# Performance work log

Measured on AMD Instinct MI355X. Metric: run time of the kernel, lower is better.

Reference implementation:

```python
import jax, jax.numpy as jnp
import numpy as np

B, S, E = 2, 2048, 2048
H, D = 16, 128  # num_attention_heads, head_dim = hidden_size // num_heads


def rotate_half(x):
    x1 = x[..., : x.shape[-1] // 2]
    x2 = x[..., x.shape[-1] // 2 :]
    return jnp.concatenate((-x2, x1), axis=-1)


def setup_inputs() -> dict:
    key = jax.random.key(0)
    ks = jax.random.split(key, 7)
    return {
        "hidden_states": jax.random.normal(ks[0], (B, S, E), dtype=jnp.float32),
        "cos": jax.random.uniform(ks[1], (1, 1, S, D), dtype=jnp.float32),
        "sin": jax.random.uniform(ks[2], (1, 1, S, D), dtype=jnp.float32),
        "wq": jax.random.normal(ks[3], (E, H * D), dtype=jnp.float32) / np.sqrt(E),
        "wk": jax.random.normal(ks[4], (E, H * D), dtype=jnp.float32) / np.sqrt(E),
        "wv": jax.random.normal(ks[5], (E, H * D), dtype=jnp.float32) / np.sqrt(E),
        "wo": jax.random.normal(ks[6], (H * D, E), dtype=jnp.float32) / np.sqrt(H * D),
    }


def reference(hidden_states, cos, sin, wq, wk, wv, wo):
    # QKV projections (no bias, per attention_bias=False)
    q = (hidden_states @ wq).reshape(B, S, H, D).transpose(0, 2, 1, 3)  # bhsd
    k = (hidden_states @ wk).reshape(B, S, H, D).transpose(0, 2, 1, 3)
    v = (hidden_states @ wv).reshape(B, S, H, D).transpose(0, 2, 1, 3)
    # RoPE (applied after the head transpose, as in the original)
    q = q * cos + rotate_half(q) * sin
    k = k * cos + rotate_half(k) * sin
    # NOTE: original forward never applies self.scaling and uses no causal mask.
    scores = jnp.einsum("bhqd,bhkd->bhqk", q, k)
    attn = jax.nn.softmax(scores.astype(jnp.float32), axis=-1)
    out = jnp.einsum("bhqk,bhkd->bhqd", attn, v)
    out = out.transpose(0, 2, 1, 3).reshape(B, S, H * D)
    return out @ wo
```

## Files before the change

### kernel.cpp

```cpp
#include <hip/hip_runtime.h>
#include <stdint.h>

typedef _Float16 f16;
typedef _Float16 half8 __attribute__((ext_vector_type(8)));
typedef _Float16 half4 __attribute__((ext_vector_type(4)));
typedef __fp16 fp16x2 __attribute__((ext_vector_type(2)));
typedef float f32x4 __attribute__((ext_vector_type(4)));
typedef float f32x16 __attribute__((ext_vector_type(16)));
typedef uint32_t u32x4 __attribute__((ext_vector_type(4)));

static constexpr int Bsz = 2, S = 2048, E = 2048, H = 16, D = 128;
static constexpr int M = Bsz * S;
static constexpr int N_QKV = 3 * H * D;
static constexpr int HD = H * D;

__device__ __forceinline__ void gload_lds16(const void* gp, void* lp) {
  __builtin_amdgcn_global_load_lds(
      (const __attribute__((address_space(1))) uint32_t*)(uintptr_t)gp,
      (__attribute__((address_space(3))) uint32_t*)(uint32_t)(uintptr_t)lp,
      16, 0, 0);
}

__device__ __forceinline__ uint32_t pkrtz(float a, float b) {
  fp16x2 r = __builtin_amdgcn_cvt_pkrtz(a, b);
  return __builtin_bit_cast(uint32_t, r);
}

__global__ void cast_f32_f16(const float* __restrict__ in, f16* __restrict__ out) {
  size_t i = (size_t)(blockIdx.x * 256 + threadIdx.x) * 8;
  float4 a = *(const float4*)&in[i];
  float4 b = *(const float4*)&in[i + 4];
  half8 h;
  h[0] = (f16)a.x; h[1] = (f16)a.y; h[2] = (f16)a.z; h[3] = (f16)a.w;
  h[4] = (f16)b.x; h[5] = (f16)b.y; h[6] = (f16)b.z; h[7] = (f16)b.w;
  *(half8*)&out[i] = h;
}

__global__ void transpose_cast(const float* __restrict__ wq, const float* __restrict__ wk,
                               const float* __restrict__ wv, const float* __restrict__ wo,
                               f16* __restrict__ wt, f16* __restrict__ wot) {
  __shared__ float tile[32][33];
  int z = blockIdx.z;
  const float* src = (z == 0) ? wq : (z == 1) ? wk : (z == 2) ? wv : wo;
  f16* dst = (z == 3) ? wot : wt + (size_t)z * E * HD;
  int bx = blockIdx.x * 32, by = blockIdx.y * 32;
  int tx = threadIdx.x, ty = threadIdx.y;
#pragma unroll
  for (int r = 0; r < 4; ++r)
    tile[ty + r * 8][tx] = src[(size_t)(by + ty + r * 8) * 2048 + bx + tx];
  __syncthreads();
#pragma unroll
  for (int r = 0; r < 4; ++r)
    dst[(size_t)(bx + ty + r * 8) * 2048 + by + tx] = (f16)tile[tx][ty + r * 8];
}

#define STAGE4(PTR, BASE, KOFF, DST)                                       \
  gload_lds16(&PTR[BASE + (KOFF) + scol], &DST[t * 8]);                    \
  gload_lds16(&PTR[BASE + (size_t)64 * Kk + (KOFF) + scol], &DST[2048 + t * 8]);

__global__ __launch_bounds__(256, 4) void qkv_fused(const f16* __restrict__ A,
                                                    const f16* __restrict__ Bt,
                                                    const float* __restrict__ cosb,
                                                    const float* __restrict__ sinb,
                                                    f16* __restrict__ Qb,
                                                    f16* __restrict__ Kb,
                                                    f16* __restrict__ VtG) {
  __shared__ f16 As[8192];
  __shared__ f16 Bs[8192];
  const int Kk = E;
  const int t = threadIdx.x, l = t & 63;
  const int wm = (t >> 7) & 1, wn = (t >> 6) & 1;
  const int lr = l & 15, g = l >> 4;
  const int bid = blockIdx.x;
  const int idx = bid >> 3;
  const int bm = (bid & 7) * 4 + (idx & 3);
  const int bn = idx >> 2;
  const int srow = t >> 2;
  const int scol = (((t & 3) ^ (srow & 3)) * 8);
  const size_t abase = (size_t)(bm * 128 + srow) * Kk;
  const size_t bbase = (size_t)(bn * 128 + srow) * Kk;
  const int bt = bn >> 4;
  const int h = bn & 15;
  const int b = bm >> 4;
  const int bh = b * 16 + h;
  const int sblk = (bm & 15) * 128;
  f32x4 acc[4][4] = {};

  if (bt < 2) {
    for (int k0 = 0; k0 < Kk; k0 += 64) {
      __syncthreads();
      STAGE4(A, abase, k0, As);
      STAGE4(Bt, bbase, k0, Bs);
      STAGE4(A, abase, k0 + 32, (As + 4096));
      STAGE4(Bt, bbase, k0 + 32, (Bs + 4096));
      __syncthreads();
#pragma unroll
      for (int kh = 0; kh < 2; ++kh) {
        const int so = kh * 4096;
        half8 af[4], bf[4];
#pragma unroll
        for (int i = 0; i < 4; ++i) {
          int ra = wm * 64 + i * 16 + lr;
          af[i] = *(const half8*)&As[so + ra * 32 + ((g ^ (ra & 3)) * 8)];
        }
#pragma unroll
        for (int j = 0; j < 4; ++j) {
          int rb = wn * 32 + (j & 1) * 16 + (j >> 1) * 64 + lr;
          bf[j] = *(const half8*)&Bs[so + rb * 32 + ((g ^ (rb & 3)) * 8)];
        }
#pragma unroll
        for (int i = 0; i < 4; ++i)
#pragma unroll
          for (int j = 0; j < 4; ++j)
            acc[i][j] = __builtin_amdgcn_mfma_f32_16x16x32_f16(bf[j], af[i], acc[i][j], 0, 0, 0);
      }
    }
    f16* Dst = (bt == 0) ? Qb : Kb;
#pragma unroll
    for (int i = 0; i < 4; ++i) {
      const int s = sblk + wm * 64 + i * 16 + lr;
      const size_t obase = ((size_t)bh * S + s) * D;
      const size_t cbase = (size_t)s * D;
#pragma unroll
      for (int j = 0; j < 2; ++j) {
        const int dlo = wn * 32 + j * 16 + g * 4;
        float4 cl = *(const float4*)&cosb[cbase + dlo];
        float4 ch = *(const float4*)&cosb[cbase + dlo + 64];
        float4 sl = *(const float4*)&sinb[cbase + dlo];
        float4 sh = *(const float4*)&sinb[cbase + dlo + 64];
        float cla[4] = {cl.x, cl.y, cl.z, cl.w}, cha[4] = {ch.x, ch.y, ch.z, ch.w};
        float sla[4] = {sl.x, sl.y, sl.z, sl.w}, sha[4] = {sh.x, sh.y, sh.z, sh.w};
        half4 olo, ohi;
#pragma unroll
        for (int r = 0; r < 4; ++r) {
          float xl = acc[i][j][r], xh = acc[i][j + 2][r];
          olo[r] = (f16)(xl * cla[r] - xh * sla[r]);
          ohi[r] = (f16)(xh * cha[r] + xl * sha[r]);
        }
        *(half4*)&Dst[obase + dlo] = olo;
        *(half4*)&Dst[obase + dlo + 64] = ohi;
      }
    }
  } else {
    for (int k0 = 0; k0 < Kk; k0 += 64) {
      __syncthreads();
      STAGE4(A, abase, k0, As);
      STAGE4(Bt, bbase, k0, Bs);
      STAGE4(A, abase, k0 + 32, (As + 4096));
      STAGE4(Bt, bbase, k0 + 32, (Bs + 4096));
      __syncthreads();
#pragma unroll
      for (int kh = 0; kh < 2; ++kh) {
        const int so = kh * 4096;
        half8 af[4], bf[4];
#pragma unroll
        for (int i = 0; i < 4; ++i) {
          int ra = wm * 64 + i * 16 + lr;
          int rb = wn * 64 + i * 16 + lr;
          af[i] = *(const half8*)&As[so + ra * 32 + ((g ^ (ra & 3)) * 8)];
          bf[i] = *(const half8*)&Bs[so + rb * 32 + ((g ^ (rb & 3)) * 8)];
        }
#pragma unroll
        for (int i = 0; i < 4; ++i)
#pragma unroll
          for (int j = 0; j < 4; ++j)
            acc[i][j] = __builtin_amdgcn_mfma_f32_16x16x32_f16(af[i], bf[j], acc[i][j], 0, 0, 0);
      }
    }
#pragma unroll
    for (int j = 0; j < 4; ++j) {
      int d = wn * 64 + j * 16 + lr;
      size_t rowb = ((size_t)bh * D + d) * S;
#pragma unroll
      for (int i = 0; i < 4; ++i) {
        int s0 = sblk + wm * 64 + i * 16 + g * 4;
        half4 h4;
#pragma unroll
        for (int r = 0; r < 4; ++r) h4[r] = (f16)acc[i][j][r];
        *(half4*)&VtG[rowb + s0] = h4;
      }
    }
  }
}

template <typename OutT>
__global__ __launch_bounds__(256, 4) void gemm_bt(const f16* __restrict__ A,
                                                  const f16* __restrict__ Bt,
                                                  OutT* __restrict__ C,
                                                  int Nn, int Kk) {
  __shared__ f16 As[8192];
  __shared__ f16 Bs[8192];
  const int t = threadIdx.x, l = t & 63;
  const int wm = (t >> 7) & 1, wn = (t >> 6) & 1;
  const int bid = blockIdx.x;
  const int bm = (bid & 7) * 4 + ((bid >> 3) & 3);
  const int bn = bid >> 5;
  const int lr = l & 15, g = l >> 4;
  const int srow = t >> 2;
  const int scol = (((t & 3) ^ (srow & 3)) * 8);
  const size_t abase = (size_t)(bm * 128 + srow) * Kk;
  const size_t bbase = (size_t)(bn * 128 + srow) * Kk;
  f32x4 acc[4][4] = {};
  for (int k0 = 0; k0 < Kk; k0 += 64) {
    __syncthreads();
    STAGE4(A, abase, k0, As);
    STAGE4(Bt, bbase, k0, Bs);
    STAGE4(A, abase, k0 + 32, (As + 4096));
    STAGE4(Bt, bbase, k0 + 32, (Bs + 4096));
    __syncthreads();
#pragma unroll
    for (int kh = 0; kh < 2; ++kh) {
      const int so = kh * 4096;
      half8 af[4], bf[4];
#pragma unroll
      for (int i = 0; i < 4; ++i) {
        int ra = wm * 64 + i * 16 + lr;
        int rb = wn * 64 + i * 16 + lr;
        af[i] = *(const half8*)&As[so + ra * 32 + ((g ^ (ra & 3)) * 8)];
        bf[i] = *(const half8*)&Bs[so + rb * 32 + ((g ^ (rb & 3)) * 8)];
      }
#pragma unroll
      for (int i = 0; i < 4; ++i)
#pragma unroll
        for (int j = 0; j < 4; ++j)
          acc[i][j] = __builtin_amdgcn_mfma_f32_16x16x32_f16(af[i], bf[j], acc[i][j], 0, 0, 0);
    }
  }
#pragma unroll
  for (int i = 0; i < 4; ++i)
#pragma unroll
    for (int j = 0; j < 4; ++j) {
      int row = bm * 128 + wm * 64 + i * 16 + g * 4;
      int col = bn * 128 + wn * 64 + j * 16 + lr;
#pragma unroll
      for (int r = 0; r < 4; ++r)
        C[(size_t)(row + r) * Nn + col] = (OutT)acc[i][j][r];
    }
}

__device__ __forceinline__ void stage_kv(const f16* __restrict__ Kg, const f16* __restrict__ Vg,
                                         f16* KsB, f16* VsB, int t, int kv) {
#pragma unroll
  for (int rnd = 0; rnd < 4; ++rnd) {
    int row = rnd * 16 + (t >> 4);
    int c = t & 15;
    gload_lds16(&Kg[(size_t)(kv + row) * D + ((c ^ (row & 7)) * 8)], &KsB[rnd * 2048 + t * 8]);
  }
#pragma unroll
  for (int rnd = 0; rnd < 4; ++rnd) {
    int row = rnd * 32 + (t >> 3);
    int c = t & 7;
    gload_lds16(&Vg[(size_t)row * S + kv + ((c ^ (row & 7)) * 8)], &VsB[rnd * 2048 + t * 8]);
  }
}

__global__ __launch_bounds__(256, 2) void flash_attn2(const f16* __restrict__ Q,
                                                      const f16* __restrict__ K,
                                                      const f16* __restrict__ Vt,
                                                      f16* __restrict__ O) {
  __shared__ f16 lds[2][16384];
  const int t = threadIdx.x, l = t & 63, w = t >> 6;
  const int c = l & 31, hi = l >> 5;
  int bid = blockIdx.x;
  bid = (bid & 7) * 64 + (bid >> 3);
  const int bh = bid >> 4, qt = bid & 15;
  const size_t baseQ = (size_t)bh * S * D;
  const f16* Kg = K + baseQ;
  const f16* Vg = Vt + (size_t)bh * D * S;
  const int q0 = qt * 128 + w * 32;
  half8 qf[8];
#pragma unroll
  for (int dc = 0; dc < 8; ++dc)
    qf[dc] = *(const half8*)&Q[baseQ + (size_t)(q0 + c) * D + dc * 16 + hi * 8];
  f32x16 o[4] = {};
  float m = -3.0e38f, ssum = 0.f;

  stage_kv(Kg, Vg, &lds[0][0], &lds[0][8192], t, 0);
  __syncthreads();

  for (int it = 0; it < S / 64; ++it) {
    const int cur = it & 1;
    const f16* KsB = &lds[cur][0];
    const f16* VsB = &lds[cur][8192];
    if (it + 1 < S / 64) stage_kv(Kg, Vg, &lds[cur ^ 1][0], &lds[cur ^ 1][8192], t, (it + 1) * 64);

    f32x16 s0 = {}, s1 = {};
    __builtin_amdgcn_s_setprio(1);
#pragma unroll
    for (int dc = 0; dc < 8; ++dc) {
      const int r0 = c, r1 = 32 + c;
      half8 kf0 = *(const half8*)&KsB[r0 * 128 + (((2 * dc + hi) ^ (r0 & 7)) * 8)];
      half8 kf1 = *(const half8*)&KsB[r1 * 128 + (((2 * dc + hi) ^ (r1 & 7)) * 8)];
      s0 = __builtin_amdgcn_mfma_f32_32x32x16_f16(kf0, qf[dc], s0, 0, 0, 0);
      s1 = __builtin_amdgcn_mfma_f32_32x32x16_f16(kf1, qf[dc], s1, 0, 0, 0);
    }
    __builtin_amdgcn_s_setprio(0);

    float tm = s0[0];
#pragma unroll
    for (int r = 1; r < 16; ++r) tm = fmaxf(tm, s0[r]);
#pragma unroll
    for (int r = 0; r < 16; ++r) tm = fmaxf(tm, s1[r]);
    tm = fmaxf(tm, __shfl_xor(tm, 32));
    if (!__all(tm <= m + 8.f)) {
      float mn = fmaxf(m, tm);
      float corr = __expf(m - mn);
      m = mn;
      ssum *= corr;
#pragma unroll
      for (int dt = 0; dt < 4; ++dt)
#pragma unroll
        for (int r = 0; r < 16; ++r) o[dt][r] *= corr;
    }
    float ts = 0.f;
#pragma unroll
    for (int r = 0; r < 16; ++r) { s0[r] = __expf(s0[r] - m); ts += s0[r]; }
#pragma unroll
    for (int r = 0; r < 16; ++r) { s1[r] = __expf(s1[r] - m); ts += s1[r]; }
    ts += __shfl_xor(ts, 32);
    ssum += ts;

    half8 pf[4];
#pragma unroll
    for (int ks = 0; ks < 4; ++ks) {
      const int B0 = 2 * (ks & 1), B1 = B0 + 1;
      uint32_t X0, X1, Y0, Y1;
      if (ks < 2) {
        X0 = pkrtz(s0[4 * B0 + 0], s0[4 * B0 + 1]);
        X1 = pkrtz(s0[4 * B0 + 2], s0[4 * B0 + 3]);
        Y0 = pkrtz(s0[4 * B1 + 0], s0[4 * B1 + 1]);
        Y1 = pkrtz(s0[4 * B1 + 2], s0[4 * B1 + 3]);
      } else {
        X0 = pkrtz(s1[4 * B0 + 0], s1[4 * B0 + 1]);
        X1 = pkrtz(s1[4 * B0 + 2], s1[4 * B0 + 3]);
        Y0 = pkrtz(s1[4 * B1 + 0], s1[4 * B1 + 1]);
        Y1 = pkrtz(s1[4 * B1 + 2], s1[4 * B1 + 3]);
      }
      asm volatile("v_permlane32_swap_b32 %0, %1" : "+v"(X0), "+v"(Y0));
      asm volatile("v_permlane32_swap_b32 %0, %1" : "+v"(X1), "+v"(Y1));
      u32x4 pw; pw[0] = X0; pw[1] = X1; pw[2] = Y0; pw[3] = Y1;
      pf[ks] = __builtin_bit_cast(half8, pw);
    }

    __builtin_amdgcn_s_setprio(1);
#pragma unroll
    for (int dt = 0; dt < 4; ++dt) {
      const int row = dt * 32 + c;
#pragma unroll
      for (int ks = 0; ks < 4; ++ks) {
        half8 vf = *(const half8*)&VsB[row * 64 + (((2 * ks + hi) ^ (row & 7)) * 8)];
        o[dt] = __builtin_amdgcn_mfma_f32_32x32x16_f16(vf, pf[ks], o[dt], 0, 0, 0);
      }
    }
    __builtin_amdgcn_s_setprio(0);
    __syncthreads();
  }

  const float inv = 1.f / ssum;
  const int b = bh >> 4, h = bh & 15;
  const size_t orow = ((size_t)(b * S + q0 + c)) * HD + h * D;
#pragma unroll
  for (int dt = 0; dt < 4; ++dt)
#pragma unroll
    for (int b2 = 0; b2 < 4; ++b2) {
      half4 h4;
#pragma unroll
      for (int a = 0; a < 4; ++a) h4[a] = (f16)(o[dt][4 * b2 + a] * inv);
      *(half4*)&O[orow + dt * 32 + 8 * b2 + 4 * hi] = h4;
    }
}

extern "C" void kernel_launch(void* const* d_in, const int* in_sizes, int n_in,
                              void* d_out, int out_size, void* d_ws, size_t ws_size,
                              hipStream_t stream) {
  (void)in_sizes; (void)n_in; (void)out_size; (void)ws_size;
  const float* hs = (const float*)d_in[0];
  const float* cosb = (const float*)d_in[1];
  const float* sinb = (const float*)d_in[2];
  const float* wq = (const float*)d_in[3];
  const float* wk = (const float*)d_in[4];
  const float* wv = (const float*)d_in[5];
  const float* wo = (const float*)d_in[6];
  float* out = (float*)d_out;
  char* ws = (char*)d_ws;
  f16* hs16 = (f16*)(ws);
  f16* attn = (f16*)(ws);
  f16* wt   = (f16*)(ws + (16u << 20));
  f16* wot  = (f16*)(ws + (40u << 20));
  f16* Qb   = (f16*)(ws + (48u << 20));
  f16* Kb   = (f16*)(ws + (64u << 20));
  f16* VtG  = (f16*)(ws + (80u << 20));

  cast_f32_f16<<<dim3(4096), dim3(256), 0, stream>>>(hs, hs16);
  transpose_cast<<<dim3(64, 64, 4), dim3(32, 8), 0, stream>>>(wq, wk, wv, wo, wt, wot);
  qkv_fused<<<dim3(1536), dim3(256), 0, stream>>>(hs16, wt, cosb, sinb, Qb, Kb, VtG);
  flash_attn2<<<dim3(512), dim3(256), 0, stream>>>(Qb, Kb, VtG, attn);
  gemm_bt<float><<<dim3(512), dim3(256), 0, stream>>>(attn, wot, out, E, HD);
}
```

Before: 274.2 us.

## Double-buffer LDS tiles in QKV and output GEMMs to overlap loads with MFMA

Both the fused QKV projection kernel and the generic GEMM now use two LDS buffers. The next K-tile is prefetched via global_load_lds while MFMAs run on the current one, and a single vmcnt wait plus barrier per iteration replaces the two __syncthreads. The aim is to hide global-memory latency behind compute. LDS use doubles to 64KB per block and the occupancy hint drops from 4 to 2 blocks per CU, which may reduce latency hiding across waves.

```diff
diff --git a/kernel.cpp b/kernel.cpp
--- a/kernel.cpp
+++ b/kernel.cpp
@@ -58,15 +58,26 @@
   gload_lds16(&PTR[BASE + (KOFF) + scol], &DST[t * 8]);                    \
   gload_lds16(&PTR[BASE + (size_t)64 * Kk + (KOFF) + scol], &DST[2048 + t * 8]);
 
-__global__ __launch_bounds__(256, 4) void qkv_fused(const f16* __restrict__ A,
+#define STAGE_TILE(k0_, bb_)                                               \
+  do {                                                                     \
+    STAGE4(A, abase, (k0_), (As + (bb_)*8192));                            \
+    STAGE4(Bt, bbase, (k0_), (Bs + (bb_)*8192));                           \
+    STAGE4(A, abase, (k0_) + 32, (As + (bb_)*8192 + 4096));                \
+    STAGE4(Bt, bbase, (k0_) + 32, (Bs + (bb_)*8192 + 4096));               \
+  } while (0)
+#define PIPE_END()                                             \
+  asm volatile("s_waitcnt vmcnt(0)" ::: "memory");             \
+  __builtin_amdgcn_s_barrier()
+
+__global__ __launch_bounds__(256, 2) void qkv_fused(const f16* __restrict__ A,
                                                     const f16* __restrict__ Bt,
                                                     const float* __restrict__ cosb,
                                                     const float* __restrict__ sinb,
                                                     f16* __restrict__ Qb,
                                                     f16* __restrict__ Kb,
                                                     f16* __restrict__ VtG) {
-  __shared__ f16 As[8192];
-  __shared__ f16 Bs[8192];
+  __shared__ f16 As[16384];
+  __shared__ f16 Bs[16384];
   const int Kk = E;
   const int t = threadIdx.x, l = t & 63;
   const int wm = (t >> 7) & 1, wn = (t >> 6) & 1;
@@ -86,17 +97,16 @@
   const int sblk = (bm & 15) * 128;
   f32x4 acc[4][4] = {};
 
+  STAGE_TILE(0, 0);
+  PIPE_END();
+
   if (bt < 2) {
-    for (int k0 = 0; k0 < Kk; k0 += 64) {
-      __syncthreads();
-      STAGE4(A, abase, k0, As);
-      STAGE4(Bt, bbase, k0, Bs);
-      STAGE4(A, abase, k0 + 32, (As + 4096));
-      STAGE4(Bt, bbase, k0 + 32, (Bs + 4096));
-      __syncthreads();
+    for (int T = 0; T < 32; ++T) {
+      const int cb = T & 1;
+      if (T + 1 < 32) STAGE_TILE((T + 1) * 64, cb ^ 1);
 #pragma unroll
       for (int kh = 0; kh < 2; ++kh) {
-        const int so = kh * 4096;
+        const int so = cb * 8192 + kh * 4096;
         half8 af[4], bf[4];
 #pragma unroll
         for (int i = 0; i < 4; ++i) {
@@ -114,6 +124,7 @@
           for (int j = 0; j < 4; ++j)
             acc[i][j] = __builtin_amdgcn_mfma_f32_16x16x32_f16(bf[j], af[i], acc[i][j], 0, 0, 0);
       }
+      if (T + 1 < 32) { PIPE_END(); }
     }
     f16* Dst = (bt == 0) ? Qb : Kb;
 #pragma unroll
@@ -142,16 +153,12 @@
       }
     }
   } else {
-    for (int k0 = 0; k0 < Kk; k0 += 64) {
-      __syncthreads();
-      STAGE4(A, abase, k0, As);
-      STAGE4(Bt, bbase, k0, Bs);
-      STAGE4(A, abase, k0 + 32, (As + 4096));
-      STAGE4(Bt, bbase, k0 + 32, (Bs + 4096));
-      __syncthreads();
+    for (int T = 0; T < 32; ++T) {
+      const int cb = T & 1;
+      if (T + 1 < 32) STAGE_TILE((T + 1) * 64, cb ^ 1);
 #pragma unroll
       for (int kh = 0; kh < 2; ++kh) {
-        const int so = kh * 4096;
+        const int so = cb * 8192 + kh * 4096;
         half8 af[4], bf[4];
 #pragma unroll
         for (int i = 0; i < 4; ++i) {
@@ -166,6 +173,7 @@
           for (int j = 0; j < 4; ++j)
             acc[i][j] = __builtin_amdgcn_mfma_f32_16x16x32_f16(af[i], bf[j], acc[i][j], 0, 0, 0);
       }
+      if (T + 1 < 32) { PIPE_END(); }
     }
 #pragma unroll
     for (int j = 0; j < 4; ++j) {
@@ -184,12 +192,12 @@
 }
 
 template <typename OutT>
-__global__ __launch_bounds__(256, 4) void gemm_bt(const f16* __restrict__ A,
+__global__ __launch_bounds__(256, 2) void gemm_bt(const f16* __restrict__ A,
                                                   const f16* __restrict__ Bt,
                                                   OutT* __restrict__ C,
                                                   int Nn, int Kk) {
-  __shared__ f16 As[8192];
-  __shared__ f16 Bs[8192];
+  __shared__ f16 As[16384];
+  __shared__ f16 Bs[16384];
   const int t = threadIdx.x, l = t & 63;
   const int wm = (t >> 7) & 1, wn = (t >> 6) & 1;
   const int bid = blockIdx.x;
@@ -201,16 +209,17 @@
   const size_t abase = (size_t)(bm * 128 + srow) * Kk;
   const size_t bbase = (size_t)(bn * 128 + srow) * Kk;
   f32x4 acc[4][4] = {};
-  for (int k0 = 0; k0 < Kk; k0 += 64) {
-    __syncthreads();
-    STAGE4(A, abase, k0, As);
-    STAGE4(Bt, bbase, k0, Bs);
-    STAGE4(A, abase, k0 + 32, (As + 4096));
-    STAGE4(Bt, bbase, k0 + 32, (Bs + 4096));
-    __syncthreads();
+  const int NT = Kk >> 6;
+
+  STAGE_TILE(0, 0);
+  PIPE_END();
+
+  for (int T = 0; T < NT; ++T) {
+    const int cb = T & 1;
+    if (T + 1 < NT) STAGE_TILE((T + 1) * 64, cb ^ 1);
 #pragma unroll
     for (int kh = 0; kh < 2; ++kh) {
-      const int so = kh * 4096;
+      const int so = cb * 8192 + kh * 4096;
       half8 af[4], bf[4];
 #pragma unroll
       for (int i = 0; i < 4; ++i) {
@@ -225,6 +234,7 @@
         for (int j = 0; j < 4; ++j)
           acc[i][j] = __builtin_amdgcn_mfma_f32_16x16x32_f16(af[i], bf[j], acc[i][j], 0, 0, 0);
     }
+    if (T + 1 < NT) { PIPE_END(); }
   }
 #pragma unroll
   for (int i = 0; i < 4; ++i)
```

After: 272.2 us. About the same (-0.7%).
